# Optimization experiments

Measured on AMD Instinct MI355X. Metric: run time of the kernel, lower is better.

## Reference

```python
import jax, jax.numpy as jnp
import numpy as np
import math

D_MODEL, HEADS, KQ = 1024, 16, 64
B, S = 2, 2048

def setup_inputs() -> dict:
    key = jax.random.key(0)
    k1, k2, k3, k4, k5 = jax.random.split(key, 5)
    scale = D_MODEL ** (-0.5)
    return {
        "x_BSE": jax.random.normal(k1, (B, S, D_MODEL), dtype=jnp.float32),
        "w_q": jax.random.normal(k2, (D_MODEL, HEADS, KQ), dtype=jnp.float32) * scale,
        "w_k": jax.random.normal(k3, (D_MODEL, HEADS, KQ), dtype=jnp.float32) * scale,
        "w_v": jax.random.normal(k4, (D_MODEL, HEADS, KQ), dtype=jnp.float32) * scale,
        "w_o": jax.random.normal(k5, (D_MODEL, HEADS, KQ), dtype=jnp.float32) * scale,
    }

def reference(x_BSE, w_q, w_k, w_v, w_o):
    # QKV projections (self-attention: memory = x)
    q_BSHK = jnp.einsum('BSE,EHK->BSHK', x_BSE, w_q)
    k_BMHK = jnp.einsum('BSE,EHK->BSHK', x_BSE, w_k)
    v_BMHK = jnp.einsum('BSE,EHK->BSHK', x_BSE, w_v)
    logits_BSHM = jnp.einsum('BSHK,BMHK->BSHM', q_BSHK, k_BMHK) / math.sqrt(KQ)
    # causal (diagonal) mask: query position >= memory position
    Sdim, Mdim = logits_BSHM.shape[1], logits_BSHM.shape[3]
    qpos = jnp.arange(Sdim)[:, None]          # [S,1]
    mpos = jnp.arange(Mdim)[None, :]          # [1,M]
    mask_SM = jnp.where(qpos >= mpos, 0.0, -jnp.inf).astype(logits_BSHM.dtype)
    logits_BSHM = logits_BSHM + mask_SM[None, :, None, :]
    probs_BSHM = jax.nn.softmax(logits_BSHM, axis=3)
    out_BSHK = jnp.einsum('BSHM,BMHK->BSHK', probs_BSHM, v_BMHK)
    return jnp.einsum('BSHK,EHK->BSE', out_BSHK, w_o)
```

## Files before the change

### kernel.cpp

```cpp
#include <hip/hip_runtime.h>
#include <hip/hip_bf16.h>

typedef __attribute__((ext_vector_type(4)))  float f32x4;
typedef __attribute__((ext_vector_type(16))) float f32x16;
typedef __attribute__((ext_vector_type(8)))  short short8;
typedef __attribute__((ext_vector_type(4)))  short short4v;

__device__ __forceinline__ short f2bf(float f) {
  union { float f; unsigned u; } x; x.f = f;
  unsigned r = (x.u + 0x7FFFu + ((x.u >> 16) & 1u)) >> 16;
  return (short)r;
}
__device__ __forceinline__ unsigned cvtpk(float lo, float hi) {
  unsigned r;
  asm("v_cvt_pk_bf16_f32 %0, %1, %2" : "=v"(r) : "v"(lo), "v"(hi));
  return r;
}
__device__ __forceinline__ void gload16(const short* g, short* l) {
  __builtin_amdgcn_global_load_lds((const __attribute__((address_space(1))) void*)g,
                                   (__attribute__((address_space(3))) void*)l, 16, 0, 0);
}

__global__ __launch_bounds__(256) void k_cast(const float* __restrict__ in,
                                              short* __restrict__ out, int n4) {
  int i = blockIdx.x * 256 + threadIdx.x;
  if (i >= n4) return;
  f32x4 v = ((const f32x4*)in)[i];
  short4v s;
  s[0] = f2bf(v[0]); s[1] = f2bf(v[1]); s[2] = f2bf(v[2]); s[3] = f2bf(v[3]);
  ((short4v*)out)[i] = s;
}

__global__ __launch_bounds__(256) void k_pack(const float* __restrict__ wq,
                                              const float* __restrict__ wk,
                                              const float* __restrict__ wv,
                                              short* __restrict__ WT) {
  int nt = blockIdx.x, et = blockIdx.y, sel = blockIdx.z;
  const float* w = sel == 0 ? wq : (sel == 1 ? wk : wv);
  __shared__ float tile[64][65];
  int tid = threadIdx.x;
  int cl = tid & 63, rw = tid >> 6;
#pragma unroll
  for (int j = 0; j < 16; ++j) {
    int el = j * 4 + rw;
    tile[el][cl] = w[(size_t)(et * 64 + el) * 1024 + nt * 64 + cl];
  }
  __syncthreads();
#pragma unroll
  for (int j = 0; j < 16; ++j) {
    int nl = j * 4 + rw;
    int n = sel * 1024 + nt * 64 + nl;
    WT[(size_t)n * 1024 + et * 64 + cl] = f2bf(tile[cl][nl]);
  }
}

template <int EPI>
__global__ __launch_bounds__(256) void k_gemm(const short* __restrict__ A,
                                              const short* __restrict__ B,
                                              short* __restrict__ Qo, short* __restrict__ Ko,
                                              short* __restrict__ Vo, float* __restrict__ out,
                                              int M, int N, int K) {
  __shared__ short As[128 * 32];
  __shared__ short Bs[128 * 32];
  int tid = threadIdx.x;
  int bm = blockIdx.y * 128, bn = blockIdx.x * 128;
  int wid = tid >> 6, lane = tid & 63;
  int wm = (wid >> 1) * 64, wn = (wid & 1) * 64;
  int lg = lane >> 4, lr = lane & 15;
  f32x4 acc[4][4] = {};

  int srow = 32 * wid + (lane >> 2);
  int schk = lane & 3;
  const short* Ag0 = A + (size_t)(bm + srow) * K + schk * 8;
  const short* Ag1 = A + (size_t)(bm + srow + 16) * K + schk * 8;
  const short* Bg0 = B + (size_t)(bn + srow) * K + schk * 8;
  const short* Bg1 = B + (size_t)(bn + srow + 16) * K + schk * 8;
  short* Al0 = &As[(32 * wid) * 32];
  short* Al1 = &As[(32 * wid + 16) * 32];
  short* Bl0 = &Bs[(32 * wid) * 32];
  short* Bl1 = &Bs[(32 * wid + 16) * 32];

  int nk = K >> 5;
  for (int kt = 0; kt < nk; ++kt) {
    int ko = kt * 32;
    __syncthreads();
    gload16(Ag0 + ko, Al0);
    gload16(Ag1 + ko, Al1);
    gload16(Bg0 + ko, Bl0);
    gload16(Bg1 + ko, Bl1);
    __syncthreads();
    short8 af[4], bf_[4];
#pragma unroll
    for (int mt = 0; mt < 4; ++mt)
      af[mt] = *(const short8*)&As[(wm + mt * 16 + lr) * 32 + lg * 8];
#pragma unroll
    for (int ntl = 0; ntl < 4; ++ntl)
      bf_[ntl] = *(const short8*)&Bs[(wn + ntl * 16 + lr) * 32 + lg * 8];
#pragma unroll
    for (int mt = 0; mt < 4; ++mt)
#pragma unroll
      for (int ntl = 0; ntl < 4; ++ntl)
        acc[mt][ntl] = __builtin_amdgcn_mfma_f32_16x16x32_bf16(af[mt], bf_[ntl], acc[mt][ntl], 0, 0, 0);
  }

#pragma unroll
  for (int mt = 0; mt < 4; ++mt)
#pragma unroll
    for (int ntl = 0; ntl < 4; ++ntl)
#pragma unroll
      for (int rr = 0; rr < 4; ++rr) {
        int m = bm + wm + mt * 16 + lg * 4 + rr;
        int n = bn + wn + ntl * 16 + lr;
        float val = acc[mt][ntl][rr];
        if (EPI == 0) {
          int b = m >> 11, s = m & 2047;
          int sel = n >> 10, hk = n & 1023;
          int h = hk >> 6, kd = hk & 63;
          if (sel == 0) Qo[((size_t)(b * 16 + h) * 2048 + s) * 64 + kd] = f2bf(val * 0.18033688011112042f);
          else if (sel == 1) Ko[((size_t)(b * 16 + h) * 2048 + s) * 64 + kd] = f2bf(val);
          else Vo[((size_t)(b * 16 + h) * 64 + kd) * 2048 + s] = f2bf(val);
        } else {
          out[(size_t)m * 1024 + n] = val;
        }
      }
}

__global__ __launch_bounds__(128, 2) void k_attn(const short* __restrict__ Q,
                                                 const short* __restrict__ K,
                                                 const short* __restrict__ VT,
                                                 short* __restrict__ O) {
  const int S = 2048;
  int bh = blockIdx.x;
  int g = 31 - blockIdx.y;

  int tid = threadIdx.x;
  int wid = tid >> 6, lane = tid & 63;
  int hi = lane >> 5, ln = lane & 31;
  int qw = 2 * g + wid;
  int ntile = qw + 1;
  int tmax = 2 * g + 2;
  int q_g = qw * 32 + ln;

  __shared__ short Ks[2][32][64];
  __shared__ short Vs[2][64][32];

  const short* Qb = Q + (size_t)bh * S * 64;
  const short* Kb = K + (size_t)bh * S * 64;
  const short* Vb = VT + (size_t)bh * 64 * S;

  short8 qf[4];
#pragma unroll
  for (int ds = 0; ds < 4; ++ds)
    qf[ds] = *(const short8*)&Qb[(size_t)q_g * 64 + ds * 16 + hi * 8];

  int kr = tid >> 2, kcb = tid & 3;
  int vd = tid >> 1, vcb = tid & 1;
  const short* kgp = Kb + (size_t)kr * 64;
  const short* vgp = Vb + (size_t)vd * S;

  short8 kreg0 = *(const short8*)&kgp[(size_t)0 + kcb * 8];
  short8 kreg1 = *(const short8*)&kgp[(size_t)0 + (kcb + 4) * 8];
  short8 vreg0 = *(const short8*)&vgp[(size_t)0 + vcb * 8];
  short8 vreg1 = *(const short8*)&vgp[(size_t)0 + (vcb + 2) * 8];

  f32x16 acoA = {}, acoB = {};
  float m = -1e30f, l = 0.f;

  for (int t = 0; t < tmax; ++t) {
    int buf = t & 1;
    *(short8*)&Ks[buf][kr][(kcb ^ (kr & 7)) * 8]       = kreg0;
    *(short8*)&Ks[buf][kr][((kcb + 4) ^ (kr & 7)) * 8] = kreg1;
    *(short8*)&Vs[buf][vd][(vcb ^ (vd & 3)) * 8]       = vreg0;
    *(short8*)&Vs[buf][vd][((vcb + 2) ^ (vd & 3)) * 8] = vreg1;
    if (t + 1 < tmax) {
      size_t ko = (size_t)(t + 1) * 32 * 64;
      size_t vo = (size_t)(t + 1) * 32;
      kreg0 = *(const short8*)&kgp[ko + kcb * 8];
      kreg1 = *(const short8*)&kgp[ko + (kcb + 4) * 8];
      vreg0 = *(const short8*)&vgp[vo + vcb * 8];
      vreg1 = *(const short8*)&vgp[vo + (vcb + 2) * 8];
    }
    __syncthreads();

    if (t < ntile) {
      short8 kc0 = *(const short8*)&Ks[buf][ln][((0 + hi) ^ (ln & 7)) * 8];
      short8 kc1 = *(const short8*)&Ks[buf][ln][((2 + hi) ^ (ln & 7)) * 8];
      short8 kc2 = *(const short8*)&Ks[buf][ln][((4 + hi) ^ (ln & 7)) * 8];
      short8 kc3 = *(const short8*)&Ks[buf][ln][((6 + hi) ^ (ln & 7)) * 8];
      f32x16 sa = {};
      __builtin_amdgcn_s_setprio(1);
      sa = __builtin_amdgcn_mfma_f32_32x32x16_bf16(kc0, qf[0], sa, 0, 0, 0);
      sa = __builtin_amdgcn_mfma_f32_32x32x16_bf16(kc1, qf[1], sa, 0, 0, 0);
      sa = __builtin_amdgcn_mfma_f32_32x32x16_bf16(kc2, qf[2], sa, 0, 0, 0);
      sa = __builtin_amdgcn_mfma_f32_32x32x16_bf16(kc3, qf[3], sa, 0, 0, 0);
      __builtin_amdgcn_s_setprio(0);

      if (t == qw) {
#pragma unroll
        for (int r = 0; r < 16; ++r) {
          int kv_g = t * 32 + (r & 3) + 8 * (r >> 2) + 4 * hi;
          if (kv_g > q_g) sa[r] = -1e30f;
        }
      }

      short8 v00 = *(const short8*)&Vs[buf][ln][((0 + hi) ^ (ln & 3)) * 8];
      short8 v01 = *(const short8*)&Vs[buf][ln][((2 + hi) ^ (ln & 3)) * 8];
      short8 v10 = *(const short8*)&Vs[buf][32 + ln][((0 + hi) ^ (ln & 3)) * 8];
      short8 v11 = *(const short8*)&Vs[buf][32 + ln][((2 + hi) ^ (ln & 3)) * 8];

      float x0 = fmaxf(sa[0], sa[1]),  x1 = fmaxf(sa[2], sa[3]);
      float x2 = fmaxf(sa[4], sa[5]),  x3 = fmaxf(sa[6], sa[7]);
      float x4 = fmaxf(sa[8], sa[9]),  x5 = fmaxf(sa[10], sa[11]);
      float x6 = fmaxf(sa[12], sa[13]), x7 = fmaxf(sa[14], sa[15]);
      x0 = fmaxf(x0, x1); x2 = fmaxf(x2, x3); x4 = fmaxf(x4, x5); x6 = fmaxf(x6, x7);
      x0 = fmaxf(x0, x2); x4 = fmaxf(x4, x6);
      float mx = fmaxf(x0, x4);
      mx = fmaxf(mx, __shfl_xor(mx, 32));

      float mnew = fmaxf(m, mx);
      float p[16];
#pragma unroll
      for (int r = 0; r < 16; ++r) p[r] = exp2f(sa[r] - mnew);
      float s0 = (p[0] + p[1]) + (p[2] + p[3]);
      float s1 = (p[4] + p[5]) + (p[6] + p[7]);
      float s2 = (p[8] + p[9]) + (p[10] + p[11]);
      float s3 = (p[12] + p[13]) + (p[14] + p[15]);
      float rsum = (s0 + s1) + (s2 + s3);
      rsum += __shfl_xor(rsum, 32);

      if (__all(mx <= m)) {
        l += rsum;
      } else {
        float alpha = exp2f(m - mnew);
        m = mnew;
        l = l * alpha + rsum;
        acoA *= alpha;
        acoB *= alpha;
      }

#pragma unroll
      for (int s = 0; s < 2; ++s) {
        unsigned c0 = cvtpk(p[8 * s + 0], p[8 * s + 1]);
        unsigned c1 = cvtpk(p[8 * s + 2], p[8 * s + 3]);
        unsigned c2 = cvtpk(p[8 * s + 4], p[8 * s + 5]);
        unsigned c3 = cvtpk(p[8 * s + 6], p[8 * s + 7]);
        unsigned pc0 = (unsigned)__shfl_xor((int)c0, 32);
        unsigned pc1 = (unsigned)__shfl_xor((int)c1, 32);
        unsigned pc2 = (unsigned)__shfl_xor((int)c2, 32);
        unsigned pc3 = (unsigned)__shfl_xor((int)c3, 32);
        union { unsigned u[4]; short8 v; } pb;
        pb.u[0] = hi ? pc2 : c0;
        pb.u[1] = hi ? pc3 : c1;
        pb.u[2] = hi ? c2 : pc0;
        pb.u[3] = hi ? c3 : pc1;
        __builtin_amdgcn_s_setprio(1);
        if (s == 0) {
          acoA = __builtin_amdgcn_mfma_f32_32x32x16_bf16(v00, pb.v, acoA, 0, 0, 0);
          acoB = __builtin_amdgcn_mfma_f32_32x32x16_bf16(v10, pb.v, acoB, 0, 0, 0);
        } else {
          acoA = __builtin_amdgcn_mfma_f32_32x32x16_bf16(v01, pb.v, acoA, 0, 0, 0);
          acoB = __builtin_amdgcn_mfma_f32_32x32x16_bf16(v11, pb.v, acoB, 0, 0, 0);
        }
        __builtin_amdgcn_s_setprio(0);
      }
    }
  }

  float rl = 1.f / l;
  int b = bh >> 4, h = bh & 15;
  size_t obase = ((size_t)b * 2048 + q_g) * 1024 + h * 64;
#pragma unroll
  for (int g4 = 0; g4 < 4; ++g4) {
    int d0 = 8 * g4 + 4 * hi;
    *(unsigned*)&O[obase + d0]          = cvtpk(acoA[4 * g4] * rl, acoA[4 * g4 + 1] * rl);
    *(unsigned*)&O[obase + d0 + 2]      = cvtpk(acoA[4 * g4 + 2] * rl, acoA[4 * g4 + 3] * rl);
    *(unsigned*)&O[obase + 32 + d0]     = cvtpk(acoB[4 * g4] * rl, acoB[4 * g4 + 1] * rl);
    *(unsigned*)&O[obase + 32 + d0 + 2] = cvtpk(acoB[4 * g4 + 2] * rl, acoB[4 * g4 + 3] * rl);
  }
}

extern "C" void kernel_launch(void* const* d_in, const int* in_sizes, int n_in,
                              void* d_out, int out_size, void* d_ws, size_t ws_size,
                              hipStream_t stream) {
  const float* x  = (const float*)d_in[0];
  const float* wq = (const float*)d_in[1];
  const float* wk = (const float*)d_in[2];
  const float* wv = (const float*)d_in[3];
  const float* wo = (const float*)d_in[4];
  float* out = (float*)d_out;
  char* ws = (char*)d_ws;

  short* x_bf  = (short*)(ws);
  short* WqkvT = (short*)(ws + ((size_t)8 << 20));
  short* wo_bf = (short*)(ws + ((size_t)14 << 20));
  short* Qb    = (short*)(ws + ((size_t)16 << 20));
  short* Kb    = (short*)(ws + ((size_t)24 << 20));
  short* Vt    = (short*)(ws + ((size_t)32 << 20));
  short* Ob    = (short*)(ws + ((size_t)40 << 20));

  k_cast<<<4096, 256, 0, stream>>>(x, x_bf, 1048576);
  k_cast<<<1024, 256, 0, stream>>>(wo, wo_bf, 262144);
  k_pack<<<dim3(16, 16, 3), 256, 0, stream>>>(wq, wk, wv, WqkvT);
  k_gemm<0><<<dim3(24, 32), 256, 0, stream>>>(x_bf, WqkvT, Qb, Kb, Vt, nullptr, 4096, 3072, 1024);
  k_attn<<<dim3(32, 32), 128, 0, stream>>>(Qb, Kb, Vt, Ob);
  k_gemm<1><<<dim3(8, 32), 256, 0, stream>>>(Ob, wo_bf, nullptr, nullptr, nullptr, out, 4096, 1024, 1024);
}
```

Baseline: 151.1 us.

## Double-buffer GEMM LDS tiles to overlap global loads with MFMA compute

Converts the shared-memory A/B tiles in the projection GEMM kernel to two buffers. The next K-slice is prefetched via global_load_lds while the current slice is computed, and the two barriers per iteration become one waitcnt plus barrier. It also raises wave priority around the MFMA block. This aims to hide global-load latency behind compute, at the cost of doubled LDS use, which may lower occupancy.

Result: faster. 143.6 us (-4.9%).

```diff
diff --git a/kernel.cpp b/kernel.cpp
--- a/kernel.cpp
+++ b/kernel.cpp
@@ -60,8 +60,8 @@
                                               short* __restrict__ Qo, short* __restrict__ Ko,
                                               short* __restrict__ Vo, float* __restrict__ out,
                                               int M, int N, int K) {
-  __shared__ short As[128 * 32];
-  __shared__ short Bs[128 * 32];
+  __shared__ short As[2][128 * 32];
+  __shared__ short Bs[2][128 * 32];
   int tid = threadIdx.x;
   int bm = blockIdx.y * 128, bn = blockIdx.x * 128;
   int wid = tid >> 6, lane = tid & 63;
@@ -75,32 +75,42 @@
   const short* Ag1 = A + (size_t)(bm + srow + 16) * K + schk * 8;
   const short* Bg0 = B + (size_t)(bn + srow) * K + schk * 8;
   const short* Bg1 = B + (size_t)(bn + srow + 16) * K + schk * 8;
-  short* Al0 = &As[(32 * wid) * 32];
-  short* Al1 = &As[(32 * wid + 16) * 32];
-  short* Bl0 = &Bs[(32 * wid) * 32];
-  short* Bl1 = &Bs[(32 * wid + 16) * 32];
+  int l0 = (32 * wid) * 32, l1 = (32 * wid + 16) * 32;
+
+  gload16(Ag0, &As[0][l0]);
+  gload16(Ag1, &As[0][l1]);
+  gload16(Bg0, &Bs[0][l0]);
+  gload16(Bg1, &Bs[0][l1]);
+  asm volatile("s_waitcnt vmcnt(0)" ::: "memory");
+  __builtin_amdgcn_s_barrier();
 
   int nk = K >> 5;
   for (int kt = 0; kt < nk; ++kt) {
-    int ko = kt * 32;
-    __syncthreads();
-    gload16(Ag0 + ko, Al0);
-    gload16(Ag1 + ko, Al1);
-    gload16(Bg0 + ko, Bl0);
-    gload16(Bg1 + ko, Bl1);
-    __syncthreads();
+    int cur = kt & 1;
+    if (kt + 1 < nk) {
+      int ko = (kt + 1) * 32;
+      int nx = cur ^ 1;
+      gload16(Ag0 + ko, &As[nx][l0]);
+      gload16(Ag1 + ko, &As[nx][l1]);
+      gload16(Bg0 + ko, &Bs[nx][l0]);
+      gload16(Bg1 + ko, &Bs[nx][l1]);
+    }
     short8 af[4], bf_[4];
 #pragma unroll
     for (int mt = 0; mt < 4; ++mt)
-      af[mt] = *(const short8*)&As[(wm + mt * 16 + lr) * 32 + lg * 8];
+      af[mt] = *(const short8*)&As[cur][(wm + mt * 16 + lr) * 32 + lg * 8];
 #pragma unroll
     for (int ntl = 0; ntl < 4; ++ntl)
-      bf_[ntl] = *(const short8*)&Bs[(wn + ntl * 16 + lr) * 32 + lg * 8];
+      bf_[ntl] = *(const short8*)&Bs[cur][(wn + ntl * 16 + lr) * 32 + lg * 8];
+    __builtin_amdgcn_s_setprio(1);
 #pragma unroll
     for (int mt = 0; mt < 4; ++mt)
 #pragma unroll
       for (int ntl = 0; ntl < 4; ++ntl)
         acc[mt][ntl] = __builtin_amdgcn_mfma_f32_16x16x32_bf16(af[mt], bf_[ntl], acc[mt][ntl], 0, 0, 0);
+    __builtin_amdgcn_s_setprio(0);
+    asm volatile("s_waitcnt vmcnt(0)" ::: "memory");
+    __builtin_amdgcn_s_barrier();
   }
 
 #pragma unroll
```
